# Kernel tuning notes

Measured on AMD Instinct MI355X. Metric: run time of the kernel, lower is better.

Reference implementation:

```python
import jax, jax.numpy as jnp
import numpy as np

B, H_IMG, W_IMG = 8, 64, 64
C, HEADS, SR, MSG = 128, 4, 4, 4
N0 = H_IMG * W_IMG


def _linear(x, w, b):
    return x @ w.T + b


def _layernorm(x, g, b, eps=1e-5):
    mu = jnp.mean(x, -1, keepdims=True)
    var = jnp.mean(jnp.square(x - mu), -1, keepdims=True)
    return (x - mu) * jax.lax.rsqrt(var + eps) * g + b


def _conv2d(x, w, b, stride, pad, groups=1):
    y = jax.lax.conv_general_dilated(
        x, w, (stride, stride), [(pad, pad), (pad, pad)],
        dimension_numbers=("NCHW", "OIHW", "NCHW"), feature_group_count=groups)
    return y + b[None, :, None, None]


def setup_inputs():
    key = jax.random.key(0)
    ks = jax.random.split(key, 16)
    def nrm(k, shape, std=0.02):
        return jax.random.normal(k, shape, jnp.float32) * std
    z = lambda *s: jnp.zeros(s, jnp.float32)
    return {
        "x": jax.random.normal(ks[0], (B, N0, C), jnp.float32),
        "msg_tokens": jax.random.normal(ks[1], (B, MSG, C), jnp.float32),
        "Wq": nrm(ks[2], (C, C)), "bq": z(C),
        "sr1_w": nrm(ks[3], (C, C, 4, 4), float(np.sqrt(2.0 / (16 * C)))), "sr1_b": z(C),
        "ln1_g": jnp.ones((C,), jnp.float32), "ln1_b": z(C),
        "sr2_w": nrm(ks[4], (C, C, 2, 2), float(np.sqrt(2.0 / (4 * C)))), "sr2_b": z(C),
        "ln2_g": jnp.ones((C,), jnp.float32), "ln2_b": z(C),
        "kv1_w": nrm(ks[5], (C, C)), "kv1_b": z(C),
        "kv2_w": nrm(ks[6], (C, C)), "kv2_b": z(C),
        "lc1_w": nrm(ks[7], (C // 2, 1, 3, 3), float(np.sqrt(2.0 / 9.0))), "lc1_b": z(C // 2),
        "lc2_w": nrm(ks[8], (C // 2, 1, 3, 3), float(np.sqrt(2.0 / 9.0))), "lc2_b": z(C // 2),
        "proj_w": nrm(ks[9], (C, C)), "proj_b": z(C),
        "H": H_IMG, "W": W_IMG,
    }


def reference(x, msg_tokens, Wq, bq, sr1_w, sr1_b, ln1_g, ln1_b,
              sr2_w, sr2_b, ln2_g, ln2_b, kv1_w, kv1_b, kv2_w, kv2_b,
              lc1_w, lc1_b, lc2_w, lc2_b, proj_w, proj_b, H, W):
    Bsz, _, Cc = x.shape
    m = msg_tokens.shape[1]
    h = HEADS
    dh = Cc // h
    scale = dh ** -0.5
    x_q = jnp.concatenate([x, msg_tokens], axis=1)       # [B, N, C]
    N = x_q.shape[1]
    q = _linear(x_q, Wq, bq).reshape(Bsz, N, h, dh).transpose(0, 2, 1, 3)  # [B,h,N,dh]
    x_img = x.transpose(0, 2, 1).reshape(Bsz, Cc, H, W)

    def branch(sr_w, sr_b, ln_g, ln_b, kv_w, kv_b, lc_w, lc_b, q_half, stride):
        Hr, Wr = H // stride, W // stride
        L = Hr * Wr
        # spatial reduction conv -> tokens
        xr = _conv2d(x_img, sr_w, sr_b, stride, 0).reshape(Bsz, Cc, L).transpose(0, 2, 1)
        # message tokens pass through the SR conv via summed weights
        msg_r = jnp.einsum('bnc,oc->bno', msg_tokens, sr_w.sum((-1, -2))) + sr_b
        xk = jax.nn.gelu(_layernorm(jnp.concatenate([xr, msg_r], 1), ln_g, ln_b), approximate=False)
        kv = _linear(xk, kv_w, kv_b).reshape(Bsz, L + m, 2, h // 2, dh).transpose(2, 0, 3, 1, 4)
        k, v = kv[0], kv[1]                               # [B, h/2, L+m, dh]
        attn = jax.nn.softmax(jnp.einsum('bhnd,bhld->bhnl', q_half, k) * scale, axis=-1)
        # fused depthwise conv on the spatial part of V (message tokens bypass)
        v_flat = v.transpose(0, 2, 1, 3).reshape(Bsz, L + m, Cc // 2).transpose(0, 2, 1)  # [B,C/2,L+m]
        lc = _conv2d(v_flat[:, :, :L].reshape(Bsz, Cc // 2, Hr, Wr), lc_w, lc_b, 1, 1,
                     groups=Cc // 2).reshape(Bsz, Cc // 2, L)
        v_add = jnp.concatenate([lc, v_flat[:, :, L:]], axis=2)
        v = v + v_add.reshape(Bsz, h // 2, dh, L + m).transpose(0, 1, 3, 2)
        return jnp.einsum('bhnl,bhld->bhnd', attn, v).transpose(0, 2, 1, 3).reshape(Bsz, N, Cc // 2)

    x1 = branch(sr1_w, sr1_b, ln1_g, ln1_b, kv1_w, kv1_b, lc1_w, lc1_b, q[:, :h // 2], SR)
    x2 = branch(sr2_w, sr2_b, ln2_g, ln2_b, kv2_w, kv2_b, lc2_w, lc2_b, q[:, h // 2:], SR // 2)
    out = _linear(jnp.concatenate([x1, x2], -1), proj_w, proj_b)
    out = x_q + out                                       # identity = x_q, drop_path = Identity
    return out[:, :-m], out[:, -m:]
```

## Files before the change

kernel.cpp:

```cpp
#include <hip/hip_runtime.h>
#include <math.h>

#define BB 8
#define CC 128
#define N0 4096
#define MSGN 4
#define NTOT 4100
#define IMG 64
#define NPAD 4160
#define LMP1 320
#define LMP2 1088

#define OFF_WFQ    0
#define OFF_WFKV1  8192
#define OFF_WFKV2  16384
#define OFF_WFPROJ 24576
#define OFF_WFSR1  32768
#define OFF_WFSR2  163840
#define OFF_QH     196608
#define OFF_XK1    2326528
#define OFF_XK2    2459648
#define OFF_KV1O   2985984
#define OFF_KV2O   3252224
#define OFF_KH1    4304896
#define OFF_VT1    4386816
#define OFF_KH2    4468736
#define OFF_VT2    4747264
#define OFF_XP     5025792

typedef _Float16 half8v __attribute__((ext_vector_type(8)));
typedef _Float16 half4v __attribute__((ext_vector_type(4)));
typedef float f32x4 __attribute__((ext_vector_type(4)));

__device__ __forceinline__ size_t af_idx(int m, int k, int Kc) {
    return ((size_t)((m >> 4) * Kc + (k >> 5)) * 64 + ((k >> 3) & 3) * 16 + (m & 15)) * 8 + (k & 7);
}

__device__ __forceinline__ float exp2_fast(float x) {
#if __has_builtin(__builtin_amdgcn_exp2f)
    return __builtin_amdgcn_exp2f(x);
#else
    return __expf(x * 0.6931471805599453f);
#endif
}

__global__ void prep_weights(const float* __restrict__ Wq, const float* __restrict__ kv1,
                             const float* __restrict__ kv2, const float* __restrict__ proj,
                             const float* __restrict__ sr1w, const float* __restrict__ sr2w,
                             float* __restrict__ ws, _Float16* __restrict__ Qh) {
    int u = blockIdx.x * blockDim.x + threadIdx.x;
    if (u >= 49152) {
        int idx = u - 49152;
        if (idx >= BB * 4 * (NPAD - NTOT) * 32) return;
        int d = idx & 31;
        int rest = idx >> 5;
        int n = NTOT + rest % (NPAD - NTOT);
        int rest2 = rest / (NPAD - NTOT);
        int hg = rest2 & 3;
        int b = rest2 >> 2;
        Qh[((size_t)(b * 4 + hg) * NPAD + n) * 32 + d] = (_Float16)0.f;
        return;
    }
    int seg, base;
    const float* w = nullptr;
    _Float16* dst;
    if (u < 2048)        { seg = 0; base = u;          w = Wq;   dst = (_Float16*)(ws + OFF_WFQ); }
    else if (u < 4096)   { seg = 0; base = u - 2048;   w = kv1;  dst = (_Float16*)(ws + OFF_WFKV1); }
    else if (u < 6144)   { seg = 0; base = u - 4096;   w = kv2;  dst = (_Float16*)(ws + OFF_WFKV2); }
    else if (u < 8192)   { seg = 0; base = u - 6144;   w = proj; dst = (_Float16*)(ws + OFF_WFPROJ); }
    else if (u < 40960)  { seg = 1; base = u - 8192;   w = sr1w; dst = (_Float16*)(ws + OFF_WFSR1); }
    else                 { seg = 2; base = u - 40960;  w = sr2w; dst = (_Float16*)(ws + OFF_WFSR2); }
    int lane = base & 63;
    int t = (base >> 6) & 7;
    int kc = base >> 9;
    int n = t * 16 + (lane & 15);
    int k0 = kc * 32 + (lane >> 4) * 8;
    half8v val;
    #pragma unroll
    for (int j = 0; j < 8; ++j) {
        int k = k0 + j;
        float v;
        if (seg == 0) v = w[n * 128 + k];
        else if (seg == 1) v = w[(n * 128 + (k & 127)) * 16 + (k >> 7)];
        else v = w[(n * 128 + (k & 127)) * 4 + (k >> 7)];
        val[j] = (_Float16)v;
    }
    *(half8v*)(dst + (size_t)base * 8) = val;
}

template<int S, int WR, int LL, int LM, int KW>
__device__ __forceinline__ void sr_partial(
    int mtile, int kcbase, int lane, const float* __restrict__ x,
    const float* __restrict__ msg, const _Float16* __restrict__ Wf, f32x4 acc[8]) {
    int m15 = lane & 15, quadk = lane >> 4;
    int m = mtile * 16 + m15;
    bool valid = m < BB * LM;
    const float* base = x;
    bool isimg = false;
    if (valid) {
        int b = m / LM, tok = m - b * LM;
        if (tok < LL) {
            int hr = tok / WR, wr = tok - hr * WR;
            base = x + ((size_t)b * N0 + hr * S * IMG + wr * S) * 128;
            isimg = true;
        } else {
            base = msg + ((size_t)b * MSGN + (tok - LL)) * 128;
        }
    }
    const half8v* Bp = (const half8v*)Wf + lane;
    for (int kk = 0; kk < KW; ++kk) {
        int kc = kcbase + kk;
        int k0 = (kc * 4 + quadk) * 8;
        int c = k0 & 127, ij = k0 >> 7;
        half8v a;
        if (valid) {
            int off;
            if (isimg) {
                int ki = ij / S, kj = ij - ki * S;
                off = (ki * IMG + kj) * 128 + c;
            } else off = c;
            const float4* p4 = (const float4*)(base + off);
            float4 f0 = p4[0], f1 = p4[1];
            a[0] = (_Float16)f0.x; a[1] = (_Float16)f0.y; a[2] = (_Float16)f0.z; a[3] = (_Float16)f0.w;
            a[4] = (_Float16)f1.x; a[5] = (_Float16)f1.y; a[6] = (_Float16)f1.z; a[7] = (_Float16)f1.w;
        } else {
            #pragma unroll
            for (int j = 0; j < 8; ++j) a[j] = (_Float16)0.f;
        }
        #pragma unroll
        for (int t = 0; t < 8; ++t)
            acc[t] = __builtin_amdgcn_mfma_f32_16x16x32_f16(a, Bp[(size_t)(kc * 8 + t) * 64], acc[t], 0, 0, 0);
    }
}

__global__ __launch_bounds__(256) void input_gemms(
    const float* __restrict__ x, const float* __restrict__ msg,
    const _Float16* __restrict__ Wf1, const _Float16* __restrict__ Wf2,
    const float* __restrict__ b1, const float* __restrict__ g1, const float* __restrict__ be1,
    const float* __restrict__ b2, const float* __restrict__ g2, const float* __restrict__ be2,
    _Float16* __restrict__ XK1, _Float16* __restrict__ XK2,
    const _Float16* __restrict__ WfQ, const float* __restrict__ bq,
    _Float16* __restrict__ Qh) {
    __shared__ float red[4][2048];
    int tid = threadIdx.x;
    int lane = tid & 63, wave = tid >> 6;
    int bid = blockIdx.x;

    if (bid >= 646) {
        int mt = (bid - 646) * 4 + wave;
        int m15 = lane & 15, quadk = lane >> 4;
        int m = mt * 16 + m15;
        bool valid = m < BB * NTOT;
        const float* rowp = x;
        if (valid) {
            int b = m / NTOT, n = m - b * NTOT;
            rowp = (n < N0) ? (x + ((size_t)b * N0 + n) * 128)
                            : (msg + ((size_t)b * MSGN + (n - N0)) * 128);
        }
        const half8v* Bp = (const half8v*)WfQ + lane;
        f32x4 acc[8];
        #pragma unroll
        for (int t = 0; t < 8; ++t) acc[t] = (f32x4){0.f, 0.f, 0.f, 0.f};
        #pragma unroll
        for (int kc = 0; kc < 4; ++kc) {
            half8v a;
            if (valid) {
                const float4* p4 = (const float4*)(rowp + (kc * 4 + quadk) * 8);
                float4 f0 = p4[0], f1 = p4[1];
                a[0] = (_Float16)f0.x; a[1] = (_Float16)f0.y; a[2] = (_Float16)f0.z; a[3] = (_Float16)f0.w;
                a[4] = (_Float16)f1.x; a[5] = (_Float16)f1.y; a[6] = (_Float16)f1.z; a[7] = (_Float16)f1.w;
            } else {
                #pragma unroll
                for (int j = 0; j < 8; ++j) a[j] = (_Float16)0.f;
            }
            #pragma unroll
            for (int t = 0; t < 8; ++t)
                acc[t] = __builtin_amdgcn_mfma_f32_16x16x32_f16(a, Bp[(size_t)(kc * 8 + t) * 64], acc[t], 0, 0, 0);
        }
        int quad = lane >> 4, n15 = lane & 15;
        const float qscale = 0.17677669529663687f * 1.4426950408889634f;
        #pragma unroll
        for (int r = 0; r < 4; ++r) {
            int mm = mt * 16 + quad * 4 + r;
            if (mm >= BB * NTOT) continue;
            int b = mm / NTOT, tok = mm - b * NTOT;
            #pragma unroll
            for (int t = 0; t < 8; ++t) {
                int n = t * 16 + n15;
                Qh[((size_t)(b * 4 + (n >> 5)) * NPAD + tok) * 32 + (n & 31)] =
                    (_Float16)((acc[t][r] + bq[n]) * qscale);
            }
        }
        return;
    }

    f32x4 acc[8];
    #pragma unroll
    for (int t = 0; t < 8; ++t) acc[t] = (f32x4){0.f, 0.f, 0.f, 0.f};
    const float* bias;
    const float* lng;
    const float* lnb;
    _Float16* outp;
    int mtile, Mv;
    if (bid < 132) {
        mtile = bid; Mv = 2080;
        sr_partial<4, 16, 256, 260, 16>(mtile, wave * 16, lane, x, msg, Wf1, acc);
        bias = b1; lng = g1; lnb = be1; outp = XK1;
    } else {
        mtile = bid - 132; Mv = 8224;
        sr_partial<2, 32, 1024, 1028, 4>(mtile, wave * 4, lane, x, msg, Wf2, acc);
        bias = b2; lng = g2; lnb = be2; outp = XK2;
    }
    int quad = lane >> 4, n15 = lane & 15;
    #pragma unroll
    for (int t = 0; t < 8; ++t)
        #pragma unroll
        for (int r = 0; r < 4; ++r)
            red[wave][(quad * 4 + r) * 128 + t * 16 + n15] = acc[t][r];
    __syncthreads();
    for (int e = tid; e < 2048; e += 256)
        red[0][e] = red[0][e] + red[1][e] + red[2][e] + red[3][e];
    __syncthreads();
    int r16 = tid >> 4, l16 = tid & 15;
    int m = mtile * 16 + r16;
    float v[8];
    float s = 0.f;
    #pragma unroll
    for (int j = 0; j < 8; ++j) { v[j] = red[0][r16 * 128 + j * 16 + l16] + bias[j * 16 + l16]; s += v[j]; }
    #pragma unroll
    for (int off = 1; off < 16; off <<= 1) s += __shfl_xor(s, off);
    float mu = s * (1.f / 128.f);
    float q = 0.f;
    #pragma unroll
    for (int j = 0; j < 8; ++j) { v[j] -= mu; q += v[j] * v[j]; }
    #pragma unroll
    for (int off = 1; off < 16; off <<= 1) q += __shfl_xor(q, off);
    float rs = rsqrtf(q * (1.f / 128.f) + 1e-5f);
    if (m < Mv) {
        #pragma unroll
        for (int j = 0; j < 8; ++j) {
            int n = j * 16 + l16;
            float y = v[j] * rs * lng[n] + lnb[n];
            y = 0.5f * y * (1.f + erff(y * 0.70710678118654752f));
            outp[af_idx(m, n, 4)] = (_Float16)y;
        }
    }
}

__global__ __launch_bounds__(256) void kv_gemm(
    const _Float16* __restrict__ XK1, const _Float16* __restrict__ XK2,
    const _Float16* __restrict__ Wf1, const _Float16* __restrict__ Wf2,
    const float* __restrict__ b1, const float* __restrict__ b2,
    float* __restrict__ o1, float* __restrict__ o2) {
    int lane = threadIdx.x & 63, wave = threadIdx.x >> 6;
    int t = blockIdx.x * 4 + wave;
    int lt;
    const half8v* Ap;
    const half8v* Bp;
    const float* bias;
    float* outp;
    if (t < 130) { lt = t;       Ap = (const half8v*)XK1 + (size_t)lt * 4 * 64 + lane; Bp = (const half8v*)Wf1 + lane; bias = b1; outp = o1; }
    else         { lt = t - 130; Ap = (const half8v*)XK2 + (size_t)lt * 4 * 64 + lane; Bp = (const half8v*)Wf2 + lane; bias = b2; outp = o2; }
    f32x4 acc[8];
    #pragma unroll
    for (int tt = 0; tt < 8; ++tt) acc[tt] = (f32x4){0.f, 0.f, 0.f, 0.f};
    #pragma unroll
    for (int kc = 0; kc < 4; ++kc) {
        half8v a = Ap[(size_t)kc * 64];
        #pragma unroll
        for (int tt = 0; tt < 8; ++tt)
            acc[tt] = __builtin_amdgcn_mfma_f32_16x16x32_f16(a, Bp[(size_t)(kc * 8 + tt) * 64], acc[tt], 0, 0, 0);
    }
    int quad = lane >> 4, n15 = lane & 15;
    #pragma unroll
    for (int r = 0; r < 4; ++r) {
        int m = lt * 16 + quad * 4 + r;
        #pragma unroll
        for (int tt = 0; tt < 8; ++tt)
            outp[(size_t)m * 128 + tt * 16 + n15] = acc[tt][r] + bias[tt * 16 + n15];
    }
}

__global__ void pack_kv(const float* __restrict__ kv1o, const float* __restrict__ kv2o,
                        const float* __restrict__ lc1w, const float* __restrict__ lc1b,
                        const float* __restrict__ lc2w, const float* __restrict__ lc2b,
                        _Float16* __restrict__ Kh1, _Float16* __restrict__ Vt1,
                        _Float16* __restrict__ Kh2, _Float16* __restrict__ Vt2) {
    int idx = blockIdx.x * 256 + threadIdx.x;
    const int T1 = BB * LMP1 * 64;
    const float* kv;
    const float* lcw;
    const float* lcb;
    _Float16* Kh;
    _Float16* Vt;
    int Wr, L, Lm, Lmp, li;
    if (idx < T1) { li = idx;      kv = kv1o; lcw = lc1w; lcb = lc1b; Kh = Kh1; Vt = Vt1; Wr = 16; L = 256;  Lm = 260;  Lmp = LMP1; }
    else          { li = idx - T1; kv = kv2o; lcw = lc2w; lcb = lc2b; Kh = Kh2; Vt = Vt2; Wr = 32; L = 1024; Lm = 1028; Lmp = LMP2; }
    int ch = li & 63;
    int rest = li >> 6;
    int n = rest % Lmp;
    int b = rest / Lmp;
    int h2 = ch >> 5, d = ch & 31;
    int Hr = L / Wr;
    float kval = 0.f, vnew = 0.f;
    if (n < Lm) {
        const float* kvb = kv + (size_t)b * Lm * 128;
        kval = kvb[(size_t)n * 128 + ch];
        float v = kvb[(size_t)n * 128 + 64 + ch];
        float add;
        if (n < L) {
            int hr = n / Wr, wr = n - hr * Wr;
            float sum = lcb[ch];
            #pragma unroll
            for (int ki = 0; ki < 3; ++ki)
                #pragma unroll
                for (int kj = 0; kj < 3; ++kj) {
                    int y = hr + ki - 1, xx = wr + kj - 1;
                    if ((unsigned)y < (unsigned)Hr && (unsigned)xx < (unsigned)Wr)
                        sum += lcw[ch * 9 + ki * 3 + kj] * kvb[((size_t)y * Wr + xx) * 128 + 64 + ch];
                }
            add = sum;
        } else {
            add = v;
        }
        vnew = v + add;
    }
    Kh[((size_t)(b * 2 + h2) * Lmp + n) * 32 + d] = (_Float16)kval;
    Vt[(size_t)(b * 2 + h2) * Lmp * 32 + (size_t)(n >> 2) * 128
       + (d & 15) * 8 + ((d >> 4) << 2) + (n & 3)] = (_Float16)vnew;
}

__global__ __launch_bounds__(128, 8) void attn_mfma(
    const _Float16* __restrict__ Qh,
    const _Float16* __restrict__ Kh1, const _Float16* __restrict__ Vt1,
    const _Float16* __restrict__ Kh2, const _Float16* __restrict__ Vt2,
    _Float16* __restrict__ XP) {
    int tid = threadIdx.x;
    int lane = tid & 63, wave = tid >> 6;
    int b = blockIdx.y;
    int z = blockIdx.z;
    int h2 = z & 1, br = 1 - (z >> 1);
    int tile = blockIdx.x * 2 + wave;
    int n0 = tile * 32;
    int q16 = lane & 15, quad = lane >> 4;
    const f32x4 zf = {0.f, 0.f, 0.f, 0.f};
    int Lmp  = br ? LMP2 : LMP1;
    int k_hi = Lmp;
    const _Float16* kb = (br ? Kh2 : Kh1) + (size_t)(b * 2 + h2) * Lmp * 32;
    const _Float16* vb = (br ? Vt2 : Vt1) + (size_t)(b * 2 + h2) * Lmp * 32;
    int hg = br * 2 + h2;
    const _Float16* qp = Qh + ((size_t)(b * 4 + hg) * NPAD + n0 + q16) * 32 + quad * 8;
    half8v qf0 = *(const half8v*)qp;
    half8v qf1 = *(const half8v*)(qp + 512);
    f32x4 O00 = zf, O01 = zf, O10 = zf, O11 = zf;
    float la = 0.f, lb = 0.f;

    half8v kf[4];
    #pragma unroll
    for (int i = 0; i < 4; ++i)
        kf[i] = *(const half8v*)(kb + (size_t)(i * 16 + q16) * 32 + quad * 8);

    for (int k0 = 0; k0 < k_hi; k0 += 64) {
        half8v vv[4];
        #pragma unroll
        for (int i = 0; i < 4; ++i)
            vv[i] = *(const half8v*)(vb + (size_t)((k0 >> 2) + i * 4 + quad) * 128 + q16 * 8);
        int k0n = (k0 + 64 < k_hi) ? k0 + 64 : 0;
        half8v kn[4];
        #pragma unroll
        for (int i = 0; i < 4; ++i)
            kn[i] = *(const half8v*)(kb + (size_t)(k0n + i * 16 + q16) * 32 + quad * 8);

        half4v p0[4], p1[4];
        #pragma unroll
        for (int i = 0; i < 4; ++i) {
            f32x4 s0 = __builtin_amdgcn_mfma_f32_16x16x32_f16(kf[i], qf0, zf, 0, 0, 0);
            f32x4 s1 = __builtin_amdgcn_mfma_f32_16x16x32_f16(kf[i], qf1, zf, 0, 0, 0);
            half4v a, c;
            #pragma unroll
            for (int r = 0; r < 4; ++r) {
                float e0 = exp2_fast(s0[r]); la += e0; a[r] = (_Float16)e0;
                float e1 = exp2_fast(s1[r]); lb += e1; c[r] = (_Float16)e1;
            }
            p0[i] = a; p1[i] = c;
        }
        #pragma unroll
        for (int i = 0; i < 4; ++i) {
            half4v v0 = __builtin_shufflevector(vv[i], vv[i], 0, 1, 2, 3);
            half4v v1 = __builtin_shufflevector(vv[i], vv[i], 4, 5, 6, 7);
            O00 = __builtin_amdgcn_mfma_f32_16x16x16f16(p0[i], v0, O00, 0, 0, 0);
            O01 = __builtin_amdgcn_mfma_f32_16x16x16f16(p0[i], v1, O01, 0, 0, 0);
            O10 = __builtin_amdgcn_mfma_f32_16x16x16f16(p1[i], v0, O10, 0, 0, 0);
            O11 = __builtin_amdgcn_mfma_f32_16x16x16f16(p1[i], v1, O11, 0, 0, 0);
        }
        #pragma unroll
        for (int i = 0; i < 4; ++i) kf[i] = kn[i];
    }

    la += __shfl_xor(la, 16); la += __shfl_xor(la, 32);
    lb += __shfl_xor(lb, 16); lb += __shfl_xor(lb, 32);
    la -= 60.0f; lb -= 60.0f;
    float ia = 1.0f / la;
    float ib = 1.0f / lb;

    int kbase = br * 64 + h2 * 32;
    #pragma unroll
    for (int r = 0; r < 4; ++r) {
        int row = quad * 4 + r;
        int src = (lane & 48) | row;
        float fa = __shfl(ia, src);
        float fb = __shfl(ib, src);
        int n = n0 + row;
        if (n < NTOT) {
            int m = b * NTOT + n;
            XP[af_idx(m, kbase + q16, 4)] = (_Float16)(O00[r] * fa);
            XP[af_idx(m, kbase + 16 + q16, 4)] = (_Float16)(O01[r] * fa);
        }
        int n2 = n + 16;
        if (n2 < NTOT) {
            int m = b * NTOT + n2;
            XP[af_idx(m, kbase + q16, 4)] = (_Float16)(O10[r] * fb);
            XP[af_idx(m, kbase + 16 + q16, 4)] = (_Float16)(O11[r] * fb);
        }
    }
}

__global__ __launch_bounds__(256) void proj_gemm(
    const _Float16* __restrict__ XP,
    const _Float16* __restrict__ Wf, const float* __restrict__ bias,
    float* __restrict__ out_f32, const float* __restrict__ x, const float* __restrict__ msg) {
    int lane = threadIdx.x & 63, wave = threadIdx.x >> 6;
    int mt = blockIdx.x * 4 + wave;
    const half8v* Ap = (const half8v*)XP + (size_t)mt * 4 * 64 + lane;
    const half8v* Bp = (const half8v*)Wf + lane;
    f32x4 acc[8];
    #pragma unroll
    for (int t = 0; t < 8; ++t) acc[t] = (f32x4){0.f, 0.f, 0.f, 0.f};
    #pragma unroll
    for (int kc = 0; kc < 4; ++kc) {
        half8v a = Ap[(size_t)kc * 64];
        #pragma unroll
        for (int t = 0; t < 8; ++t)
            acc[t] = __builtin_amdgcn_mfma_f32_16x16x32_f16(a, Bp[(size_t)(kc * 8 + t) * 64], acc[t], 0, 0, 0);
    }
    int quad = lane >> 4, n15 = lane & 15;
    #pragma unroll
    for (int r = 0; r < 4; ++r) {
        int m = mt * 16 + quad * 4 + r;
        if (m >= BB * NTOT) continue;
        int b = m / NTOT, tok = m - b * NTOT;
        const float* rp;
        float* dst;
        if (tok < N0) {
            rp = x + ((size_t)b * N0 + tok) * 128;
            dst = out_f32 + ((size_t)b * N0 + tok) * 128;
        } else {
            rp = msg + ((size_t)b * MSGN + (tok - N0)) * 128;
            dst = out_f32 + (size_t)BB * N0 * 128 + ((size_t)b * MSGN + (tok - N0)) * 128;
        }
        #pragma unroll
        for (int t = 0; t < 8; ++t) {
            int n = t * 16 + n15;
            dst[n] = acc[t][r] + bias[n] + rp[n];
        }
    }
}

extern "C" void kernel_launch(void* const* d_in, const int* in_sizes, int n_in,
                              void* d_out, int out_size, void* d_ws, size_t ws_size,
                              hipStream_t stream) {
    const float* x     = (const float*)d_in[0];
    const float* msg   = (const float*)d_in[1];
    const float* Wq    = (const float*)d_in[2];
    const float* bq    = (const float*)d_in[3];
    const float* sr1w  = (const float*)d_in[4];
    const float* sr1b  = (const float*)d_in[5];
    const float* ln1g  = (const float*)d_in[6];
    const float* ln1b  = (const float*)d_in[7];
    const float* sr2w  = (const float*)d_in[8];
    const float* sr2b  = (const float*)d_in[9];
    const float* ln2g  = (const float*)d_in[10];
    const float* ln2b  = (const float*)d_in[11];
    const float* kv1w  = (const float*)d_in[12];
    const float* kv1b  = (const float*)d_in[13];
    const float* kv2w  = (const float*)d_in[14];
    const float* kv2b  = (const float*)d_in[15];
    const float* lc1w  = (const float*)d_in[16];
    const float* lc1b  = (const float*)d_in[17];
    const float* lc2w  = (const float*)d_in[18];
    const float* lc2b  = (const float*)d_in[19];
    const float* projw = (const float*)d_in[20];
    const float* projb = (const float*)d_in[21];
    float* ws  = (float*)d_ws;
    float* out = (float*)d_out;

    _Float16* WfQ    = (_Float16*)(ws + OFF_WFQ);
    _Float16* WfKV1  = (_Float16*)(ws + OFF_WFKV1);
    _Float16* WfKV2  = (_Float16*)(ws + OFF_WFKV2);
    _Float16* WfPROJ = (_Float16*)(ws + OFF_WFPROJ);
    _Float16* WfSR1  = (_Float16*)(ws + OFF_WFSR1);
    _Float16* WfSR2  = (_Float16*)(ws + OFF_WFSR2);
    _Float16* Qh     = (_Float16*)(ws + OFF_QH);
    _Float16* XP     = (_Float16*)(ws + OFF_XP);
    _Float16* XK1    = (_Float16*)(ws + OFF_XK1);
    _Float16* XK2    = (_Float16*)(ws + OFF_XK2);
    float* kv1o      = ws + OFF_KV1O;
    float* kv2o      = ws + OFF_KV2O;
    _Float16* Kh1    = (_Float16*)(ws + OFF_KH1);
    _Float16* Vt1    = (_Float16*)(ws + OFF_VT1);
    _Float16* Kh2    = (_Float16*)(ws + OFF_KH2);
    _Float16* Vt2    = (_Float16*)(ws + OFF_VT2);

    prep_weights<<<432, 256, 0, stream>>>(Wq, kv1w, kv2w, projw, sr1w, sr2w, ws, Qh);
    input_gemms<<<1159, 256, 0, stream>>>(x, msg, WfSR1, WfSR2,
                                          sr1b, ln1g, ln1b, sr2b, ln2g, ln2b,
                                          XK1, XK2, WfQ, bq, Qh);
    kv_gemm<<<161, 256, 0, stream>>>(XK1, XK2, WfKV1, WfKV2, kv1b, kv2b, kv1o, kv2o);
    pack_kv<<<2816, 256, 0, stream>>>(kv1o, kv2o, lc1w, lc1b, lc2w, lc2b,
                                      Kh1, Vt1, Kh2, Vt2);
    attn_mfma<<<dim3(65, 8, 4), 128, 0, stream>>>(Qh, Kh1, Vt1, Kh2, Vt2, XP);
    proj_gemm<<<513, 256, 0, stream>>>(XP, WfPROJ, projb, out, x, msg);
}
```

Measured before the change: 226.1 us.

## Stage K/V tiles through LDS with async global_load_lds double buffering

The attention kernel now uses 4-wave blocks that cooperatively copy each 64-key K and V tile into shared memory with global_load_lds. The copies are double buffered, so the next tile loads while the current one computes, and a barrier closes each iteration. Before, each wave loaded K/V straight from global memory with register prefetch. Sharing the tiles across waves is meant to cut redundant global/L2 traffic. The query padding grows to fit the larger tile, so the workspace offsets and the padding-zeroing grid change too, and the per-iteration __syncthreads adds synchronisation cost.

```diff
diff --git a/kernel.cpp b/kernel.cpp
--- a/kernel.cpp
+++ b/kernel.cpp
@@ -7,7 +7,7 @@
 #define MSGN 4
 #define NTOT 4100
 #define IMG 64
-#define NPAD 4160
+#define NPAD 4224
 #define LMP1 320
 #define LMP2 1088
 
@@ -18,15 +18,15 @@
 #define OFF_WFSR1  32768
 #define OFF_WFSR2  163840
 #define OFF_QH     196608
-#define OFF_XK1    2326528
-#define OFF_XK2    2459648
-#define OFF_KV1O   2985984
-#define OFF_KV2O   3252224
-#define OFF_KH1    4304896
-#define OFF_VT1    4386816
-#define OFF_KH2    4468736
-#define OFF_VT2    4747264
-#define OFF_XP     5025792
+#define OFF_XK1    2359296
+#define OFF_XK2    2492416
+#define OFF_KV1O   3018752
+#define OFF_KV2O   3284992
+#define OFF_KH1    4337664
+#define OFF_VT1    4419584
+#define OFF_KH2    4501504
+#define OFF_VT2    4780032
+#define OFF_XP     5058560
 
 typedef _Float16 half8v __attribute__((ext_vector_type(8)));
 typedef _Float16 half4v __attribute__((ext_vector_type(4)));
@@ -42,6 +42,12 @@
 #else
     return __expf(x * 0.6931471805599453f);
 #endif
+}
+
+__device__ __forceinline__ void gload16(const _Float16* g, _Float16* l) {
+    __builtin_amdgcn_global_load_lds(
+        (const __attribute__((address_space(1))) unsigned int*)g,
+        (__attribute__((address_space(3))) unsigned int*)l, 16, 0, 0);
 }
 
 __global__ void prep_weights(const float* __restrict__ Wq, const float* __restrict__ kv1,
@@ -330,22 +336,24 @@
        + (d & 15) * 8 + ((d >> 4) << 2) + (n & 3)] = (_Float16)vnew;
 }
 
-__global__ __launch_bounds__(128, 8) void attn_mfma(
+__global__ __launch_bounds__(256, 4) void attn_mfma(
     const _Float16* __restrict__ Qh,
     const _Float16* __restrict__ Kh1, const _Float16* __restrict__ Vt1,
     const _Float16* __restrict__ Kh2, const _Float16* __restrict__ Vt2,
     _Float16* __restrict__ XP) {
+    __shared__ _Float16 sK[2][2048];
+    __shared__ _Float16 sV[2][2048];
     int tid = threadIdx.x;
     int lane = tid & 63, wave = tid >> 6;
     int b = blockIdx.y;
     int z = blockIdx.z;
     int h2 = z & 1, br = 1 - (z >> 1);
-    int tile = blockIdx.x * 2 + wave;
+    int tile = blockIdx.x * 4 + wave;
     int n0 = tile * 32;
     int q16 = lane & 15, quad = lane >> 4;
     const f32x4 zf = {0.f, 0.f, 0.f, 0.f};
-    int Lmp  = br ? LMP2 : LMP1;
-    int k_hi = Lmp;
+    int NT = br ? (LMP2 / 64) : (LMP1 / 64);
+    int Lmp = br ? LMP2 : LMP1;
     const _Float16* kb = (br ? Kh2 : Kh1) + (size_t)(b * 2 + h2) * Lmp * 32;
     const _Float16* vb = (br ? Vt2 : Vt1) + (size_t)(b * 2 + h2) * Lmp * 32;
     int hg = br * 2 + h2;
@@ -355,21 +363,27 @@
     f32x4 O00 = zf, O01 = zf, O10 = zf, O11 = zf;
     float la = 0.f, lb = 0.f;
 
-    half8v kf[4];
-    #pragma unroll
-    for (int i = 0; i < 4; ++i)
-        kf[i] = *(const half8v*)(kb + (size_t)(i * 16 + q16) * 32 + quad * 8);
-
-    for (int k0 = 0; k0 < k_hi; k0 += 64) {
-        half8v vv[4];
+    int ksrc = (wave * 16 + q16) * 32 + quad * 8;
+    int vsrc = wave * 512 + lane * 8;
+
+    gload16(kb + ksrc, &sK[0][wave * 512]);
+    gload16(vb + vsrc, &sV[0][wave * 512]);
+    __syncthreads();
+
+    for (int t = 0; t < NT; ++t) {
+        int cur = t & 1;
+        if (t + 1 < NT) {
+            size_t o = (size_t)(t + 1) * 2048;
+            gload16(kb + o + ksrc, &sK[cur ^ 1][wave * 512]);
+            gload16(vb + o + vsrc, &sV[cur ^ 1][wave * 512]);
+        }
+        half8v kf[4], vv[4];
         #pragma unroll
         for (int i = 0; i < 4; ++i)
-            vv[i] = *(const half8v*)(vb + (size_t)((k0 >> 2) + i * 4 + quad) * 128 + q16 * 8);
-        int k0n = (k0 + 64 < k_hi) ? k0 + 64 : 0;
-        half8v kn[4];
+            kf[i] = *(const half8v*)&sK[cur][i * 512 + lane * 8];
         #pragma unroll
         for (int i = 0; i < 4; ++i)
-            kn[i] = *(const half8v*)(kb + (size_t)(k0n + i * 16 + q16) * 32 + quad * 8);
+            vv[i] = *(const half8v*)&sV[cur][i * 512 + quad * 128 + q16 * 8];
 
         half4v p0[4], p1[4];
         #pragma unroll
@@ -393,8 +407,7 @@
             O10 = __builtin_amdgcn_mfma_f32_16x16x16f16(p1[i], v0, O10, 0, 0, 0);
             O11 = __builtin_amdgcn_mfma_f32_16x16x16f16(p1[i], v1, O11, 0, 0, 0);
         }
-        #pragma unroll
-        for (int i = 0; i < 4; ++i) kf[i] = kn[i];
+        __syncthreads();
     }
 
     la += __shfl_xor(la, 16); la += __shfl_xor(la, 32);
@@ -511,13 +524,13 @@
     _Float16* Kh2    = (_Float16*)(ws + OFF_KH2);
     _Float16* Vt2    = (_Float16*)(ws + OFF_VT2);
 
-    prep_weights<<<432, 256, 0, stream>>>(Wq, kv1w, kv2w, projw, sr1w, sr2w, ws, Qh);
+    prep_weights<<<688, 256, 0, stream>>>(Wq, kv1w, kv2w, projw, sr1w, sr2w, ws, Qh);
     input_gemms<<<1159, 256, 0, stream>>>(x, msg, WfSR1, WfSR2,
                                           sr1b, ln1g, ln1b, sr2b, ln2g, ln2b,
                                           XK1, XK2, WfQ, bq, Qh);
     kv_gemm<<<161, 256, 0, stream>>>(XK1, XK2, WfKV1, WfKV2, kv1b, kv2b, kv1o, kv2o);
     pack_kv<<<2816, 256, 0, stream>>>(kv1o, kv2o, lc1w, lc1b, lc2w, lc2b,
                                       Kh1, Vt1, Kh2, Vt2);
-    attn_mfma<<<dim3(65, 8, 4), 128, 0, stream>>>(Qh, Kh1, Vt1, Kh2, Vt2, XP);
+    attn_mfma<<<dim3(33, 8, 4), 256, 0, stream>>>(Qh, Kh1, Vt1, Kh2, Vt2, XP);
     proj_gemm<<<513, 256, 0, stream>>>(XP, WfPROJ, projb, out, x, msg);
 }
```

Result: faster. 191.0 us (-15.5%).
